# Optimization experiments

Measured on AMD Instinct MI355X. Metric: run time of the kernel, lower is better.

Reference implementation:

```python
import jax, jax.numpy as jnp
import numpy as np

N_USER = 1_000_000
N_ITEM = 100_000
E = 16          # embedding_size
O = 16          # out_size per head
H = 4           # head_num
HID = 32        # hidden_size
B = 8192        # batch
S = 200         # sample_num
L = 50          # history length
NSUPP = 50_000  # supp_user_num


def _xavier(key, shape):
    fan_in, fan_out = shape[-2], shape[-1]
    std = np.sqrt(2.0 / (fan_in + fan_out))
    return (jax.random.normal(key, shape) * std).astype(jnp.float32)


def setup_inputs() -> dict:
    key = jax.random.key(0)
    ks = jax.random.split(key, 16)
    uid = jax.random.randint(ks[0], (B,), 0, N_USER)
    iid = jax.random.randint(ks[1], (B,), 0, N_ITEM)
    return {
        "user_embedding": _xavier(ks[2], (N_USER, E)),
        "item_embedding": _xavier(ks[3], (N_ITEM, E)),
        "wq": _xavier(ks[4], (H, E, O)),   # per-head Wq (no bias)
        "wk": _xavier(ks[5], (H, E, O)),
        "wv": _xavier(ks[6], (H, O, O)),
        "w_out": _xavier(ks[7], (H * O, O)),
        "l1_w": _xavier(ks[8], (3 * E, HID)),
        "l1_b": jnp.full((HID,), 0.1, jnp.float32),
        "l2_w": _xavier(ks[9], (HID, HID // 2)),
        "l2_b": jnp.full((HID // 2,), 0.1, jnp.float32),
        "l3_w": _xavier(ks[10], (HID // 2, 1)),
        "l3_b": jnp.full((1,), 0.1, jnp.float32),
        "user_bias": jnp.zeros((N_USER, 1), jnp.float32),
        "item_bias": jnp.zeros((N_ITEM, 1), jnp.float32),
        "x": jnp.stack([uid, iid], axis=1),                          # [B,2]
        "history": jax.random.randint(ks[11], (B, L), 0, N_ITEM),    # [B,L]
        "history_len": jax.random.randint(ks[12], (B,), 1, L + 1),   # [B] >=1
        "supp_users": jax.random.randint(ks[13], (NSUPP,), 0, N_USER),
        "sample_index": jax.random.randint(ks[14], (H, B, S), 0, NSUPP),
    }


def reference(user_embedding, item_embedding, wq, wk, wv, w_out,
              l1_w, l1_b, l2_w, l2_b, l3_w, l3_b, user_bias, item_bias,
              x, history, history_len, supp_users, sample_index):
    user_id = x[:, 0]
    item_id = x[:, 1]

    # user init embedding = mean-by-len of full (unmasked) history, as in source
    hist_emb = item_embedding[history]                                # [B,L,E]
    user_init = hist_emb.sum(axis=1) / history_len[:, None].astype(jnp.float32)  # [B,E]

    # per-head GAT over sampled support users (all heads vectorized)
    nb = user_embedding[supp_users[sample_index]]                     # [H,B,S,E]
    q = jnp.einsum('be,heo->hbo', user_init, wq)                      # [H,B,O]
    k = jnp.einsum('hbse,heo->hbso', nb, wk)                          # [H,B,S,O]
    attn = jax.nn.softmax(jnp.einsum('hbo,hbso->hbs', q, k), axis=-1)
    ctx = jnp.einsum('hbs,hbso->hbo', attn, k)                        # [H,B,O]
    gat = jnp.einsum('hbo,hop->hbp', ctx, wv)                         # [H,B,O]
    gat = jnp.transpose(gat, (1, 0, 2)).reshape(B, H * O)             # concat heads

    user_emb = gat @ w_out                                            # [B,O]
    item_emb = item_embedding[item_id]                                # [B,E]
    interaction = user_emb * item_emb
    ratings = interaction.sum(axis=1)

    h = jnp.concatenate([user_emb, item_emb, interaction], axis=1)    # [B,3E]
    x1 = jnp.tanh(h @ l1_w + l1_b)
    x2 = jnp.tanh(x1 @ l2_w + l2_b)
    x3 = (x2 @ l3_w + l3_b).reshape(-1)

    ub = user_bias[user_id, 0]
    ib = item_bias[item_id, 0]
    return (ratings + x3) / 2.0 + ub + ib
```

## Files before the change

kernel.cpp:

```cpp
#include <hip/hip_runtime.h>
#include <math.h>

#define N_USERS 1000000
#define N_ITEMS 100000
#define EMB 16
#define OUTD 16
#define NH 4
#define HID 32
#define BB 8192
#define SS 200
#define LL 50
#define NSUPP 50000

typedef float v4f __attribute__((ext_vector_type(4)));
typedef _Float16 h2 __attribute__((ext_vector_type(2)));
typedef _Float16 h4 __attribute__((ext_vector_type(4)));

#define WAVE_SYNC() do { asm volatile("s_waitcnt lgkmcnt(0)" ::: "memory"); \
                         __builtin_amdgcn_sched_barrier(0); } while (0)

__global__ __launch_bounds__(256) void prep_kernel(
    const float* __restrict__ user_emb,
    const int*   __restrict__ supp_users,
    const float* __restrict__ wk,
    const float* __restrict__ wq,
    const float* __restrict__ wv,
    const float* __restrict__ item_emb,
    const int*   __restrict__ history,
    const int*   __restrict__ history_len,
    _Float16*    __restrict__ tbl,
    _Float16*    __restrict__ qtbuf,
    float*       __restrict__ Wkv)
{
    __shared__ float s_ui[4][EMB];
    __shared__ float s_wq[NH * EMB * OUTD];
    __shared__ float s_wk[NH * EMB * OUTD];
    __shared__ float s_q[4][NH * OUTD];

    int t = threadIdx.x;
    if (blockIdx.x < NSUPP / 16) {
        int n0 = blockIdx.x * 16;
        int ul = t >> 4, e = t & 15;
        int row = supp_users[n0 + ul];
        tbl[(size_t)(n0 + ul) * EMB + e] =
            (_Float16)user_emb[(size_t)row * EMB + e];
    } else if (blockIdx.x < NSUPP / 16 + BB / 4) {
        for (int i = t; i < NH * EMB * OUTD; i += 256) {
            s_wq[i] = wq[i];
            s_wk[i] = wk[i];
        }
        int g    = t >> 6;
        int lane = t & 63;
        int l4   = lane >> 4;
        int e    = lane & 15;
        int b    = (blockIdx.x - NSUPP / 16) * 4 + g;

        float sum = 0.f;
        for (int l = l4; l < LL; l += 4) {
            int it = __builtin_nontemporal_load(history + (size_t)b * LL + l);
            sum += item_emb[(size_t)it * EMB + e];
        }
        sum += __shfl_xor(sum, 16);
        sum += __shfl_xor(sum, 32);
        if (lane < EMB) s_ui[g][lane] = sum / (float)history_len[b];
        __syncthreads();

        int h = (t >> 4) & 3;
        int o = t & 15;
        float acc = 0.f;
#pragma unroll
        for (int ee = 0; ee < EMB; ++ee)
            acc += s_ui[g][ee] * s_wq[(h * EMB + ee) * OUTD + o];
        s_q[g][h * OUTD + o] = acc;
        __syncthreads();

        float qt = 0.f;
#pragma unroll
        for (int oo = 0; oo < OUTD; ++oo)
            qt += s_wk[(h * EMB + o) * OUTD + oo] * s_q[g][h * OUTD + oo];
        qtbuf[((size_t)b * NH + h) * EMB + o] = (_Float16)qt;
    } else {
        for (int i = t; i < NH * EMB * OUTD; i += 256) {
            int h = i >> 8, e = (i >> 4) & 15, p = i & 15;
            float a = 0.f;
#pragma unroll
            for (int o = 0; o < OUTD; ++o)
                a += wk[(h * EMB + e) * OUTD + o] * wv[(h * OUTD + o) * OUTD + p];
            Wkv[i] = a;
        }
    }
}

__global__ __launch_bounds__(256, 4) void attn_epi_kernel(
    const _Float16* __restrict__ tbl,
    const _Float16* __restrict__ qtbuf,
    const int*   __restrict__ sample_index,
    const float* __restrict__ Wkv,
    const float* __restrict__ item_emb,
    const float* __restrict__ w_out,
    const float* __restrict__ l1_w, const float* __restrict__ l1_b,
    const float* __restrict__ l2_w, const float* __restrict__ l2_b,
    const float* __restrict__ l3_w, const float* __restrict__ l3_b,
    const float* __restrict__ user_bias, const float* __restrict__ item_bias,
    const int*   __restrict__ x,
    float*       __restrict__ out)
{
    __shared__ float s_gat[4][NH * OUTD];
    __shared__ float s_ue[4][OUTD];
    __shared__ float s_ie[4][EMB];
    __shared__ float s_x1[4][HID];
    __shared__ float s_x2[4][HID / 2];

    int h    = threadIdx.x >> 6;
    int lane = threadIdx.x & 63;
    int g    = lane >> 2;
    int qt   = lane & 3;

    const h4* U4 = (const h4*)tbl;

    for (int bl = 0; bl < 4; ++bl) {
        int b = blockIdx.x * 4 + bl;

        const int* si = sample_index + ((size_t)h * BB + b) * SS;
        int pre0 = __builtin_nontemporal_load(si + lane);
        int pre1 = __builtin_nontemporal_load(si + lane + 64);
        int pre2 = __builtin_nontemporal_load(si + lane + 128);
        int pre3 = (lane < 8) ? __builtin_nontemporal_load(si + lane + 192) : 0;

        h4 qh = ((const h4*)(qtbuf + ((size_t)b * NH + h) * EMB))[qt];
        h2 qlo = {qh.x, qh.y};
        h2 qhi = {qh.z, qh.w};

        int idx[13];
#pragma unroll
        for (int r = 0; r < 13; ++r) {
            int pre = (r < 4) ? pre0 : (r < 8) ? pre1 : (r < 12) ? pre2 : pre3;
            idx[r] = __shfl(pre, (r & 3) * 16 + g, 64);
        }

        h4 kq[13];
#pragma unroll
        for (int r = 0; r < 13; ++r)
            kq[r] = U4[(size_t)idx[r] * 4 + qt];

        float l = 0.f;
        v4f c = {0.f, 0.f, 0.f, 0.f};
#pragma unroll
        for (int r = 0; r < 13; ++r) {
            h2 klo = {kq[r].x, kq[r].y};
            h2 khi = {kq[r].z, kq[r].w};
            float p = __builtin_amdgcn_fdot2(klo, qlo,
                      __builtin_amdgcn_fdot2(khi, qhi, 0.f, false), false);
            p += __shfl_xor(p, 1);
            p += __shfl_xor(p, 2);
            float w = __expf(p);
            if (r == 12) w = (g < 8) ? w : 0.f;
            l += w;
            c += w * __builtin_convertvector(kq[r], v4f);
        }
#pragma unroll
        for (int off = 4; off < 64; off <<= 1) {
            l   += __shfl_xor(l, off);
            c.x += __shfl_xor(c.x, off);
            c.y += __shfl_xor(c.y, off);
            c.z += __shfl_xor(c.z, off);
            c.w += __shfl_xor(c.w, off);
        }
        float inv = 1.f / l;

        float part = c.x * Wkv[((size_t)h * EMB + qt * 4 + 0) * OUTD + g]
                   + c.y * Wkv[((size_t)h * EMB + qt * 4 + 1) * OUTD + g]
                   + c.z * Wkv[((size_t)h * EMB + qt * 4 + 2) * OUTD + g]
                   + c.w * Wkv[((size_t)h * EMB + qt * 4 + 3) * OUTD + g];
        part += __shfl_xor(part, 1);
        part += __shfl_xor(part, 2);
        if (qt == 0)
            s_gat[bl][h * OUTD + g] = part * inv;
    }
    __syncthreads();

    int b   = blockIdx.x * 4 + h;
    int uid = x[(size_t)b * 2 + 0];
    int iid = x[(size_t)b * 2 + 1];

    if (lane < EMB) s_ie[h][lane] = item_emb[(size_t)iid * EMB + lane];
    if (lane < OUTD) {
        float acc = 0.f;
#pragma unroll
        for (int j = 0; j < NH * OUTD; ++j)
            acc += s_gat[h][j] * w_out[j * OUTD + lane];
        s_ue[h][lane] = acc;
    }
    WAVE_SYNC();

    if (lane < HID) {
        float acc = l1_b[lane];
#pragma unroll
        for (int i = 0; i < EMB; ++i) {
            float ue = s_ue[h][i], ie = s_ie[h][i];
            acc += ue * l1_w[i * HID + lane]
                 + ie * l1_w[(EMB + i) * HID + lane]
                 + ue * ie * l1_w[(2 * EMB + i) * HID + lane];
        }
        s_x1[h][lane] = tanhf(acc);
    }
    WAVE_SYNC();

    if (lane < HID / 2) {
        float acc = l2_b[lane];
#pragma unroll
        for (int j = 0; j < HID; ++j)
            acc += s_x1[h][j] * l2_w[j * (HID / 2) + lane];
        s_x2[h][lane] = tanhf(acc);
    }
    WAVE_SYNC();

    if (lane == 0) {
        float x3 = l3_b[0];
#pragma unroll
        for (int j = 0; j < HID / 2; ++j) x3 += s_x2[h][j] * l3_w[j];
        float ratings = 0.f;
#pragma unroll
        for (int o = 0; o < OUTD; ++o) ratings += s_ue[h][o] * s_ie[h][o];
        out[b] = 0.5f * (ratings + x3) + user_bias[uid] + item_bias[iid];
    }
}

extern "C" void kernel_launch(void* const* d_in, const int* in_sizes, int n_in,
                              void* d_out, int out_size, void* d_ws, size_t ws_size,
                              hipStream_t stream) {
    const float* user_embedding = (const float*)d_in[0];
    const float* item_embedding = (const float*)d_in[1];
    const float* wq             = (const float*)d_in[2];
    const float* wk             = (const float*)d_in[3];
    const float* wv             = (const float*)d_in[4];
    const float* w_out          = (const float*)d_in[5];
    const float* l1_w           = (const float*)d_in[6];
    const float* l1_b           = (const float*)d_in[7];
    const float* l2_w           = (const float*)d_in[8];
    const float* l2_b           = (const float*)d_in[9];
    const float* l3_w           = (const float*)d_in[10];
    const float* l3_b           = (const float*)d_in[11];
    const float* user_bias      = (const float*)d_in[12];
    const float* item_bias      = (const float*)d_in[13];
    const int*   x              = (const int*)d_in[14];
    const int*   history        = (const int*)d_in[15];
    const int*   history_len    = (const int*)d_in[16];
    const int*   supp_users     = (const int*)d_in[17];
    const int*   sample_index   = (const int*)d_in[18];
    float* out = (float*)d_out;

    char* ws = (char*)d_ws;
    _Float16* tbl = (_Float16*)ws;
    ws += (size_t)NSUPP * EMB * sizeof(_Float16);
    _Float16* qtbuf = (_Float16*)ws;
    ws += (size_t)BB * NH * EMB * sizeof(_Float16);
    float* Wkv = (float*)ws;

    prep_kernel<<<NSUPP / 16 + BB / 4 + 1, 256, 0, stream>>>(
        user_embedding, supp_users, wk, wq, wv,
        item_embedding, history, history_len, tbl, qtbuf, Wkv);
    attn_epi_kernel<<<BB / 4, 256, 0, stream>>>(
        tbl, qtbuf, sample_index, Wkv, item_embedding, w_out,
        l1_w, l1_b, l2_w, l2_b, l3_w, l3_b,
        user_bias, item_bias, x, out);
}
```

Before: 201.2 us.

## Fuse user-init and query projection into attention kernel, drop qtbuf round-trip

The history mean-pooling and the q/Wk projection move out of the prep kernel and into the attention/epilogue kernel. Each wave computes the transformed query for its batch row into shared memory, so the fp16 qtbuf no longer goes through global memory. The prep grid shrinks to just the support-table gather and the Wkv block. The cost is a larger shared-memory footprint and extra prologue latency per attention block, which may lower occupancy at launch bounds (256,4).

```diff
diff --git a/kernel.cpp b/kernel.cpp
--- a/kernel.cpp
+++ b/kernel.cpp
@@ -23,20 +23,10 @@
     const float* __restrict__ user_emb,
     const int*   __restrict__ supp_users,
     const float* __restrict__ wk,
-    const float* __restrict__ wq,
     const float* __restrict__ wv,
-    const float* __restrict__ item_emb,
-    const int*   __restrict__ history,
-    const int*   __restrict__ history_len,
     _Float16*    __restrict__ tbl,
-    _Float16*    __restrict__ qtbuf,
     float*       __restrict__ Wkv)
 {
-    __shared__ float s_ui[4][EMB];
-    __shared__ float s_wq[NH * EMB * OUTD];
-    __shared__ float s_wk[NH * EMB * OUTD];
-    __shared__ float s_q[4][NH * OUTD];
-
     int t = threadIdx.x;
     if (blockIdx.x < NSUPP / 16) {
         int n0 = blockIdx.x * 16;
@@ -44,41 +34,6 @@
         int row = supp_users[n0 + ul];
         tbl[(size_t)(n0 + ul) * EMB + e] =
             (_Float16)user_emb[(size_t)row * EMB + e];
-    } else if (blockIdx.x < NSUPP / 16 + BB / 4) {
-        for (int i = t; i < NH * EMB * OUTD; i += 256) {
-            s_wq[i] = wq[i];
-            s_wk[i] = wk[i];
-        }
-        int g    = t >> 6;
-        int lane = t & 63;
-        int l4   = lane >> 4;
-        int e    = lane & 15;
-        int b    = (blockIdx.x - NSUPP / 16) * 4 + g;
-
-        float sum = 0.f;
-        for (int l = l4; l < LL; l += 4) {
-            int it = __builtin_nontemporal_load(history + (size_t)b * LL + l);
-            sum += item_emb[(size_t)it * EMB + e];
-        }
-        sum += __shfl_xor(sum, 16);
-        sum += __shfl_xor(sum, 32);
-        if (lane < EMB) s_ui[g][lane] = sum / (float)history_len[b];
-        __syncthreads();
-
-        int h = (t >> 4) & 3;
-        int o = t & 15;
-        float acc = 0.f;
-#pragma unroll
-        for (int ee = 0; ee < EMB; ++ee)
-            acc += s_ui[g][ee] * s_wq[(h * EMB + ee) * OUTD + o];
-        s_q[g][h * OUTD + o] = acc;
-        __syncthreads();
-
-        float qt = 0.f;
-#pragma unroll
-        for (int oo = 0; oo < OUTD; ++oo)
-            qt += s_wk[(h * EMB + o) * OUTD + oo] * s_q[g][h * OUTD + oo];
-        qtbuf[((size_t)b * NH + h) * EMB + o] = (_Float16)qt;
     } else {
         for (int i = t; i < NH * EMB * OUTD; i += 256) {
             int h = i >> 8, e = (i >> 4) & 15, p = i & 15;
@@ -93,10 +48,13 @@
 
 __global__ __launch_bounds__(256, 4) void attn_epi_kernel(
     const _Float16* __restrict__ tbl,
-    const _Float16* __restrict__ qtbuf,
     const int*   __restrict__ sample_index,
     const float* __restrict__ Wkv,
+    const float* __restrict__ wq,
+    const float* __restrict__ wk,
     const float* __restrict__ item_emb,
+    const int*   __restrict__ history,
+    const int*   __restrict__ history_len,
     const float* __restrict__ w_out,
     const float* __restrict__ l1_w, const float* __restrict__ l1_b,
     const float* __restrict__ l2_w, const float* __restrict__ l2_b,
@@ -105,16 +63,59 @@
     const int*   __restrict__ x,
     float*       __restrict__ out)
 {
-    __shared__ float s_gat[4][NH * OUTD];
-    __shared__ float s_ue[4][OUTD];
-    __shared__ float s_ie[4][EMB];
-    __shared__ float s_x1[4][HID];
-    __shared__ float s_x2[4][HID / 2];
-
-    int h    = threadIdx.x >> 6;
-    int lane = threadIdx.x & 63;
-    int g    = lane >> 2;
-    int qt   = lane & 3;
+    __shared__ float    s_wq[NH * EMB * OUTD];
+    __shared__ float    s_wk[NH * EMB * OUTD];
+    __shared__ float    s_ui[4][EMB];
+    __shared__ float    s_q[4][NH * OUTD];
+    __shared__ _Float16 s_qt[4][NH][EMB];
+    __shared__ float    s_gat[4][NH * OUTD];
+    __shared__ float    s_ue[4][OUTD];
+    __shared__ float    s_ie[4][EMB];
+    __shared__ float    s_x1[4][HID];
+    __shared__ float    s_x2[4][HID / 2];
+
+    int tid  = threadIdx.x;
+    int wv64 = tid >> 6;
+    int lane = tid & 63;
+
+    for (int i = tid; i < NH * EMB * OUTD; i += 256) {
+        s_wq[i] = wq[i];
+        s_wk[i] = wk[i];
+    }
+    {
+        int b  = blockIdx.x * 4 + wv64;
+        int l4 = lane >> 4;
+        int e  = lane & 15;
+        float sum = 0.f;
+        for (int l = l4; l < LL; l += 4) {
+            int it = __builtin_nontemporal_load(history + (size_t)b * LL + l);
+            sum += item_emb[(size_t)it * EMB + e];
+        }
+        sum += __shfl_xor(sum, 16);
+        sum += __shfl_xor(sum, 32);
+        if (lane < EMB) s_ui[wv64][lane] = sum / (float)history_len[b];
+        WAVE_SYNC();
+
+        int h = lane >> 4;
+        int o = lane & 15;
+        float acc = 0.f;
+#pragma unroll
+        for (int ee = 0; ee < EMB; ++ee)
+            acc += s_ui[wv64][ee] * s_wq[(h * EMB + ee) * OUTD + o];
+        s_q[wv64][h * OUTD + o] = acc;
+        WAVE_SYNC();
+
+        float qt = 0.f;
+#pragma unroll
+        for (int oo = 0; oo < OUTD; ++oo)
+            qt += s_wk[(h * EMB + o) * OUTD + oo] * s_q[wv64][h * OUTD + oo];
+        s_qt[wv64][h][o] = (_Float16)qt;
+    }
+    __syncthreads();
+
+    int h  = wv64;
+    int g  = lane >> 2;
+    int qt = lane & 3;
 
     const h4* U4 = (const h4*)tbl;
 
@@ -127,7 +128,7 @@
         int pre2 = __builtin_nontemporal_load(si + lane + 128);
         int pre3 = (lane < 8) ? __builtin_nontemporal_load(si + lane + 192) : 0;
 
-        h4 qh = ((const h4*)(qtbuf + ((size_t)b * NH + h) * EMB))[qt];
+        h4 qh = ((const h4*)&s_qt[bl][h][0])[qt];
         h2 qlo = {qh.x, qh.y};
         h2 qhi = {qh.z, qh.w};
 
@@ -253,15 +254,13 @@
     char* ws = (char*)d_ws;
     _Float16* tbl = (_Float16*)ws;
     ws += (size_t)NSUPP * EMB * sizeof(_Float16);
-    _Float16* qtbuf = (_Float16*)ws;
-    ws += (size_t)BB * NH * EMB * sizeof(_Float16);
     float* Wkv = (float*)ws;
 
-    prep_kernel<<<NSUPP / 16 + BB / 4 + 1, 256, 0, stream>>>(
-        user_embedding, supp_users, wk, wq, wv,
-        item_embedding, history, history_len, tbl, qtbuf, Wkv);
+    prep_kernel<<<NSUPP / 16 + 1, 256, 0, stream>>>(
+        user_embedding, supp_users, wk, wv, tbl, Wkv);
     attn_epi_kernel<<<BB / 4, 256, 0, stream>>>(
-        tbl, qtbuf, sample_index, Wkv, item_embedding, w_out,
+        tbl, sample_index, Wkv, wq, wk,
+        item_embedding, history, history_len, w_out,
         l1_w, l1_b, l2_w, l2_b, l3_w, l3_b,
         user_bias, item_bias, x, out);
 }
```

New measurement: 204.3 us. No clear change (+1.5%).
